# Kernel tuning notes

Measured on AMD Instinct MI355X. Metric: run time of the kernel, lower is better.

## Reference

```python
import jax, jax.numpy as jnp
import numpy as np

N_NODES = 50000
N_EDGES = 800000
IN_DIM = 128
OUT_DIM = 128
CLASS_NUM = 40
EPS = 0.0  # PyG GINConv default eps


def setup_inputs() -> dict:
    key = jax.random.key(0)
    k1, k2, k3, k4 = jax.random.split(key, 4)
    x = jax.random.normal(k1, (N_NODES, IN_DIM), dtype=jnp.float32)
    edge_index = jax.random.randint(k2, (2, N_EDGES), 0, N_NODES, dtype=jnp.int64)
    # Linear(in, out, bias=False) weights, torch layout [out, in]
    W1 = jax.random.normal(k3, (OUT_DIM, IN_DIM), dtype=jnp.float32) / np.sqrt(IN_DIM)
    W2 = jax.random.normal(k4, (CLASS_NUM, OUT_DIM), dtype=jnp.float32) / np.sqrt(OUT_DIM)
    return {"x": x, "edge_index": edge_index, "W1": W1, "W2": W2}


def gin_conv(x, edge_index, W):
    # GINConv: nn((1+eps)*x + sum_{j in N(i)} x_j)
    src, dst = edge_index[0], edge_index[1]
    agg = jax.ops.segment_sum(x[src], dst, num_segments=x.shape[0])  # [N, d]
    h = (1.0 + EPS) * x + agg
    return h @ W.T


def reference(x, edge_index, W1, W2):
    # Layer 1 + relu (dropout is identity at inference, p=0.5 only in training)
    h = jax.nn.relu(gin_conv(x, edge_index, W1))
    # Layer 2 (logits)
    out = gin_conv(h, edge_index, W2)
    return out
```

## Files before the change

kernel.cpp:

```cpp
#include <hip/hip_runtime.h>

#define N_NODES 50000
#define N_EDGES 800000
#define BSHIFT 6
#define NBKT   ((N_NODES + 63) >> BSHIFT)
#define CAP    2048
#define CHUNK_EDGES 4096
#define NBIN_BLOCKS ((N_EDGES + CHUNK_EDGES - 1) / CHUNK_EDGES)
#define NB32   ((N_NODES + 31) / 32)
#define N_PAD  50048
#define GEMM1_NB ((N_NODES + 63) / 64)

typedef __attribute__((ext_vector_type(8))) short short8;
typedef __attribute__((ext_vector_type(4))) float f32x4;

__device__ __forceinline__ int load_idx(const void* ei, int is64, long long pos) {
  return is64 ? (int)((const long long*)ei)[pos] : ((const int*)ei)[pos];
}

__device__ __forceinline__ unsigned bfr(float f) {
  unsigned u = __float_as_uint(f);
  return (u + 0x7FFFu + ((u >> 16) & 1u)) >> 16;
}
__device__ __forceinline__ unsigned bfpk(float lo, float hi) {
  return bfr(lo) | (bfr(hi) << 16);
}
#define ACC_BF4(acc, u)                                                    \
  acc.x += __uint_as_float((u).x << 16);                                   \
  acc.y += __uint_as_float((u).x & 0xffff0000u);                           \
  acc.z += __uint_as_float((u).y << 16);                                   \
  acc.w += __uint_as_float((u).y & 0xffff0000u);

__global__ __launch_bounds__(256) void prep_kernel(const float* __restrict__ W1,
                                                   const float* __restrict__ W2,
                                                   int* __restrict__ resv,
                                                   unsigned short* __restrict__ W1bf,
                                                   unsigned short* __restrict__ W2bf) {
  int b = blockIdx.x, tid = threadIdx.x;
  if (b == 0) {
    ((int4*)resv)[tid] = make_int4(0, 0, 0, 0);
    return;
  }
  int j = (b - 1) * 256 + tid;
  if (j < 128 * 128) {
    W1bf[j] = (unsigned short)bfr(W1[j]);
  } else {
    int jj = j - 128 * 128;
    int c = jj >> 7, k = jj & 127;
    W2bf[jj] = (c < 40) ? (unsigned short)bfr(W2[c * 128 + k]) : 0;
  }
}

__global__ __launch_bounds__(256) void binPlace2_kernel(const void* __restrict__ ei,
                                                        int* __restrict__ resv,
                                                        unsigned* __restrict__ binned) {
  __shared__ int cnt[NBKT];
  __shared__ int lbase[NBKT];
  __shared__ int sflag;
  int tid = threadIdx.x;
  if (tid < 64) {
    const long long* e64 = (const long long*)ei;
    long long v = e64[tid];
    unsigned long long m = __ballot(v >= 0 && v < N_NODES);
    if (tid == 0) sflag = (m == ~0ull) ? 1 : 0;
  }
  for (int i = tid; i < NBKT; i += 256) cnt[i] = 0;
  __syncthreads();
  int f = sflag;
  long long base = (long long)blockIdx.x * CHUNK_EDGES;
  unsigned pk[CHUNK_EDGES / 256];
  #pragma unroll
  for (int it = 0; it < CHUNK_EDGES / 256; ++it) {
    long long e = base + it * 256 + tid;
    unsigned p = 0xFFFFFFFFu;
    if (e < N_EDGES) {
      int src = load_idx(ei, f, e);
      int dst = load_idx(ei, f, (long long)N_EDGES + e);
      int bk = dst >> BSHIFT;
      p = (unsigned)src | ((unsigned)(dst & 63) << 16) | ((unsigned)bk << 22);
      atomicAdd(&cnt[bk], 1);
    }
    pk[it] = p;
  }
  __syncthreads();
  for (int i = tid; i < NBKT; i += 256) {
    int c = cnt[i];
    lbase[i] = c ? (i * CAP + atomicAdd(&resv[i], c)) : 0;
    cnt[i] = 0;
  }
  __syncthreads();
  #pragma unroll
  for (int it = 0; it < CHUNK_EDGES / 256; ++it) {
    unsigned p = pk[it];
    if (p != 0xFFFFFFFFu) {
      int bk = p >> 22;
      int off = atomicAdd(&cnt[bk], 1);
      binned[lbase[bk] + off] = p & 0x3FFFFFu;
    }
  }
}

__global__ __launch_bounds__(256) void csr_gemm1_kernel(const unsigned* __restrict__ binned,
                                                        const int* __restrict__ resv,
                                                        int* __restrict__ rowptr,
                                                        unsigned short* __restrict__ col,
                                                        const float* __restrict__ xin,
                                                        const unsigned short* __restrict__ W1bf,
                                                        unsigned short* __restrict__ Ysbf) {
  __shared__ unsigned short Ysh[64 * 128];
  __shared__ int red[256];
  __shared__ int ncnt[64];
  __shared__ int ncur[64];
  int tid = threadIdx.x;

  if (blockIdx.x < NBKT) {
    int b = blockIdx.x;
    int s = 0;
    for (int i = tid; i < b; i += 256) s += resv[i];
    red[tid] = s;
    __syncthreads();
    #pragma unroll
    for (int off = 128; off > 0; off >>= 1) {
      if (tid < off) red[tid] += red[tid + off];
      __syncthreads();
    }
    int gb = red[0];
    int c = resv[b];
    if (tid < 64) ncnt[tid] = 0;
    if (b == 0 && tid == 0) rowptr[N_NODES] = N_EDGES;
    __syncthreads();
    const unsigned* bb = binned + (size_t)b * CAP;
    for (int i = tid; i < c; i += 256)
      atomicAdd(&ncnt[(bb[i] >> 16) & 63], 1);
    __syncthreads();
    if (tid == 0) {
      int a = gb;
      #pragma unroll
      for (int j = 0; j < 64; ++j) { int t = ncnt[j]; ncur[j] = a; a += t; }
    }
    __syncthreads();
    int node0 = b << BSHIFT;
    if (tid < 64 && node0 + tid < N_NODES) rowptr[node0 + tid] = ncur[tid];
    __syncthreads();
    for (int i = tid; i < c; i += 256) {
      unsigned p = bb[i];
      int slot = atomicAdd(&ncur[(p >> 16) & 63], 1);
      col[slot] = (unsigned short)(p & 0xFFFFu);
    }
    return;
  }

  int wave = tid >> 6, lane = tid & 63;
  int rl = lane & 15, kg = lane >> 4;
  int n0 = (blockIdx.x - NBKT) * 64;
  int rowg = n0 + wave * 16 + rl;
  int row = (rowg < N_NODES) ? rowg : (N_NODES - 1);
  f32x4 acc[8];
  #pragma unroll
  for (int t = 0; t < 8; ++t) acc[t] = (f32x4)(0.f);
  #pragma unroll
  for (int kk = 0; kk < 4; ++kk) {
    int k0 = kk * 32 + kg * 8;
    const float* xr = xin + (size_t)row * 128 + k0;
    float4 a0 = *(const float4*)xr;
    float4 a1 = *(const float4*)(xr + 4);
    short8 a;
    a[0] = (short)bfr(a0.x); a[1] = (short)bfr(a0.y);
    a[2] = (short)bfr(a0.z); a[3] = (short)bfr(a0.w);
    a[4] = (short)bfr(a1.x); a[5] = (short)bfr(a1.y);
    a[6] = (short)bfr(a1.z); a[7] = (short)bfr(a1.w);
    #pragma unroll
    for (int t = 0; t < 8; ++t) {
      short8 b = *(const short8*)(W1bf + (t * 16 + rl) * 128 + k0);
      acc[t] = __builtin_amdgcn_mfma_f32_16x16x32_bf16(a, b, acc[t], 0, 0, 0);
    }
  }
  #pragma unroll
  for (int t = 0; t < 8; ++t) {
    #pragma unroll
    for (int reg = 0; reg < 4; ++reg)
      Ysh[(wave * 16 + kg * 4 + reg) * 128 + t * 16 + rl] =
          (unsigned short)bfr(acc[t][reg]);
  }
  __syncthreads();
  int rows = N_NODES - n0; if (rows > 64) rows = 64;
  uint4* dstb = (uint4*)Ysbf;
  const uint4* srcb = (const uint4*)Ysh;
  for (int i = tid; i < rows * 16; i += 256) {
    int r = i >> 4, j = i & 15;
    int slice = j >> 2, q = j & 3;
    dstb[(size_t)slice * (N_PAD * 4) + (size_t)(n0 + r) * 4 + q] = srcb[i];
  }
}

__global__ __launch_bounds__(256) void gather1_kernel(const unsigned short* __restrict__ Ys,
                                                      const int* __restrict__ rowptr,
                                                      const unsigned short* __restrict__ col,
                                                      unsigned short* __restrict__ h1bf) {
  int bid = blockIdx.x;
  int slice = bid / NB32;
  int nb = bid - slice * NB32;
  int lane = threadIdx.x & 63;
  int wv = threadIdx.x >> 6;
  int g = lane >> 3, s = lane & 7;
  int w = nb * 32 + wv * 8 + g;
  if (w >= N_NODES) return;
  const uint2* Y2 = (const uint2*)(Ys + (size_t)slice * N_PAD * 32);
  float4 acc = make_float4(0.f, 0.f, 0.f, 0.f);
  {
    uint2 u = Y2[(size_t)w * 8 + s];
    ACC_BF4(acc, u);
  }
  int i = rowptr[w], end = rowptr[w + 1];
  for (; i + 3 < end; i += 4) {
    int s0 = col[i], s1 = col[i + 1], s2 = col[i + 2], s3 = col[i + 3];
    uint2 u0 = Y2[(size_t)s0 * 8 + s];
    uint2 u1 = Y2[(size_t)s1 * 8 + s];
    uint2 u2 = Y2[(size_t)s2 * 8 + s];
    uint2 u3 = Y2[(size_t)s3 * 8 + s];
    ACC_BF4(acc, u0); ACC_BF4(acc, u1); ACC_BF4(acc, u2); ACC_BF4(acc, u3);
  }
  for (; i < end; ++i) {
    uint2 u = Y2[(size_t)col[i] * 8 + s];
    ACC_BF4(acc, u);
  }
  uint2 p;
  p.x = bfpk(fmaxf(acc.x, 0.f), fmaxf(acc.y, 0.f));
  p.y = bfpk(fmaxf(acc.z, 0.f), fmaxf(acc.w, 0.f));
  ((uint2*)h1bf)[(size_t)w * 32 + slice * 8 + s] = p;
}

__global__ __launch_bounds__(256) void gather2_kernel(const unsigned short* __restrict__ Zbf,
                                                      const int* __restrict__ rowptr,
                                                      const unsigned short* __restrict__ col,
                                                      float* __restrict__ outp) {
  int lane = threadIdx.x & 63;
  int wv = threadIdx.x >> 6;
  int g = lane >> 3, s = lane & 7;
  int w = blockIdx.x * 32 + wv * 8 + g;
  if (w >= N_NODES) return;
  const uint2* Z2 = (const uint2*)Zbf;
  bool ex = s < 2;
  float4 acc = make_float4(0.f, 0.f, 0.f, 0.f);
  float4 acc2 = make_float4(0.f, 0.f, 0.f, 0.f);
  {
    uint2 u = Z2[(size_t)w * 10 + s];
    ACC_BF4(acc, u);
    if (ex) { uint2 v = Z2[(size_t)w * 10 + 8 + s]; ACC_BF4(acc2, v); }
  }
  int i = rowptr[w], end = rowptr[w + 1];
  for (; i + 1 < end; i += 2) {
    int s0 = col[i], s1 = col[i + 1];
    uint2 u0 = Z2[(size_t)s0 * 10 + s];
    uint2 u1 = Z2[(size_t)s1 * 10 + s];
    ACC_BF4(acc, u0); ACC_BF4(acc, u1);
    if (ex) {
      uint2 v0 = Z2[(size_t)s0 * 10 + 8 + s];
      uint2 v1 = Z2[(size_t)s1 * 10 + 8 + s];
      ACC_BF4(acc2, v0); ACC_BF4(acc2, v1);
    }
  }
  for (; i < end; ++i) {
    int s0 = col[i];
    uint2 u0 = Z2[(size_t)s0 * 10 + s];
    ACC_BF4(acc, u0);
    if (ex) { uint2 v0 = Z2[(size_t)s0 * 10 + 8 + s]; ACC_BF4(acc2, v0); }
  }
  float4* o4 = (float4*)(outp + (size_t)w * 40);
  o4[s] = acc;
  if (ex) o4[8 + s] = acc2;
}

__global__ __launch_bounds__(256) void gemm2_kernel(const unsigned short* __restrict__ h1bf,
                                                    const unsigned short* __restrict__ W2bf,
                                                    unsigned short* __restrict__ Zbf) {
  __shared__ unsigned short Zsh[64 * 40];
  int tid = threadIdx.x;
  int wave = tid >> 6, lane = tid & 63;
  int rl = lane & 15, kg = lane >> 4;
  int n0 = blockIdx.x * 64;
  int rowg = n0 + wave * 16 + rl;
  int row = (rowg < N_NODES) ? rowg : (N_NODES - 1);
  f32x4 acc[3];
  #pragma unroll
  for (int t = 0; t < 3; ++t) acc[t] = (f32x4)(0.f);
  #pragma unroll
  for (int kk = 0; kk < 4; ++kk) {
    int k0 = kk * 32 + kg * 8;
    short8 a = *(const short8*)(h1bf + (size_t)row * 128 + k0);
    #pragma unroll
    for (int t = 0; t < 3; ++t) {
      short8 b = *(const short8*)(W2bf + (t * 16 + rl) * 128 + k0);
      acc[t] = __builtin_amdgcn_mfma_f32_16x16x32_bf16(a, b, acc[t], 0, 0, 0);
    }
  }
  #pragma unroll
  for (int t = 0; t < 3; ++t) {
    int c = t * 16 + rl;
    if (c < 40) {
      #pragma unroll
      for (int reg = 0; reg < 4; ++reg)
        Zsh[(wave * 16 + kg * 4 + reg) * 40 + c] = (unsigned short)bfr(acc[t][reg]);
    }
  }
  __syncthreads();
  int rows = N_NODES - n0; if (rows > 64) rows = 64;
  unsigned* dst = (unsigned*)Zbf + (size_t)n0 * 20;
  const unsigned* src = (const unsigned*)Zsh;
  for (int i = tid; i < rows * 20; i += 256) dst[i] = src[i];
}

extern "C" void kernel_launch(void* const* d_in, const int* in_sizes, int n_in,
                              void* d_out, int out_size, void* d_ws, size_t ws_size,
                              hipStream_t stream) {
  const float* x  = (const float*)d_in[0];
  const void*  ei = d_in[1];
  const float* W1 = (const float*)d_in[2];
  const float* W2 = (const float*)d_in[3];
  float* out = (float*)d_out;

  int* resv   = (int*)d_ws;
  int* rowptr = resv + 1024;
  unsigned* binned = (unsigned*)(rowptr + 50176);
  unsigned short* col  = (unsigned short*)(binned + (size_t)NBKT * CAP);
  unsigned short* Ysbf = col + N_EDGES;
  unsigned short* h1bf = Ysbf + (size_t)4 * N_PAD * 32;
  unsigned short* W1bf = h1bf + (size_t)N_NODES * 128;
  unsigned short* W2bf = W1bf + 128 * 128;
  unsigned short* Zbf  = Ysbf;

  prep_kernel<<<89, 256, 0, stream>>>(W1, W2, resv, W1bf, W2bf);
  binPlace2_kernel<<<NBIN_BLOCKS, 256, 0, stream>>>(ei, resv, binned);
  csr_gemm1_kernel<<<NBKT + GEMM1_NB, 256, 0, stream>>>(binned, resv, rowptr, col,
                                                        x, W1bf, Ysbf);
  gather1_kernel<<<4 * NB32, 256, 0, stream>>>(Ysbf, rowptr, col, h1bf);
  gemm2_kernel<<<GEMM1_NB, 256, 0, stream>>>(h1bf, W2bf, Zbf);
  gather2_kernel<<<NB32, 256, 0, stream>>>(Zbf, rowptr, col, out);
}
```

Baseline: 116.6 us.

## Sort nodes by degree within 128-node buckets to balance gather work

```diff
diff --git a/kernel.cpp b/kernel.cpp
--- a/kernel.cpp
+++ b/kernel.cpp
@@ -2,12 +2,14 @@
 
 #define N_NODES 50000
 #define N_EDGES 800000
-#define BSHIFT 6
-#define NBKT   ((N_NODES + 63) >> BSHIFT)
-#define CAP    2048
+#define BSHIFT 7
+#define BKT_NODES 128
+#define NBKT   ((N_NODES + BKT_NODES - 1) >> BSHIFT)
+#define CAP    4096
 #define CHUNK_EDGES 4096
 #define NBIN_BLOCKS ((N_EDGES + CHUNK_EDGES - 1) / CHUNK_EDGES)
-#define NB32   ((N_NODES + 31) / 32)
+#define NPERM  (NBKT * BKT_NODES)
+#define NB32P  (NPERM / 32)
 #define N_PAD  50048
 #define GEMM1_NB ((N_NODES + 63) / 64)
 
@@ -25,11 +27,11 @@
 __device__ __forceinline__ unsigned bfpk(float lo, float hi) {
   return bfr(lo) | (bfr(hi) << 16);
 }
-#define ACC_BF4(acc, u)                                                    \
+#define ACC_BF4F(acc, u)                                                   \
   acc.x += __uint_as_float((u).x << 16);                                   \
-  acc.y += __uint_as_float((u).x & 0xffff0000u);                           \
+  acc.y += __uint_as_float((u).x);                                         \
   acc.z += __uint_as_float((u).y << 16);                                   \
-  acc.w += __uint_as_float((u).y & 0xffff0000u);
+  acc.w += __uint_as_float((u).y);
 
 __global__ __launch_bounds__(256) void prep_kernel(const float* __restrict__ W1,
                                                    const float* __restrict__ W2,
@@ -77,7 +79,7 @@
       int src = load_idx(ei, f, e);
       int dst = load_idx(ei, f, (long long)N_EDGES + e);
       int bk = dst >> BSHIFT;
-      p = (unsigned)src | ((unsigned)(dst & 63) << 16) | ((unsigned)bk << 22);
+      p = (unsigned)src | ((unsigned)(dst & 127) << 16) | ((unsigned)bk << 23);
       atomicAdd(&cnt[bk], 1);
     }
     pk[it] = p;
@@ -93,9 +95,9 @@
   for (int it = 0; it < CHUNK_EDGES / 256; ++it) {
     unsigned p = pk[it];
     if (p != 0xFFFFFFFFu) {
-      int bk = p >> 22;
+      int bk = p >> 23;
       int off = atomicAdd(&cnt[bk], 1);
-      binned[lbase[bk] + off] = p & 0x3FFFFFu;
+      binned[lbase[bk] + off] = p & 0x7FFFFFu;
     }
   }
 }
@@ -104,13 +106,16 @@
                                                         const int* __restrict__ resv,
                                                         int* __restrict__ rowptr,
                                                         unsigned short* __restrict__ col,
+                                                        unsigned short* __restrict__ permw,
                                                         const float* __restrict__ xin,
                                                         const unsigned short* __restrict__ W1bf,
                                                         unsigned short* __restrict__ Ysbf) {
   __shared__ unsigned short Ysh[64 * 128];
   __shared__ int red[256];
-  __shared__ int ncnt[64];
-  __shared__ int ncur[64];
+  __shared__ int ncnt[BKT_NODES];
+  __shared__ int ncur[BKT_NODES];
+  __shared__ int dcnt[64];
+  __shared__ int dcur[64];
   int tid = threadIdx.x;
 
   if (blockIdx.x < NBKT) {
@@ -126,25 +131,43 @@
     }
     int gb = red[0];
     int c = resv[b];
-    if (tid < 64) ncnt[tid] = 0;
+    if (tid < BKT_NODES) ncnt[tid] = 0;
+    if (tid < 64) dcnt[tid] = 0;
+    if (tid < BKT_NODES) permw[(size_t)b * BKT_NODES + tid] = 0xFFFFu;
     if (b == 0 && tid == 0) rowptr[N_NODES] = N_EDGES;
     __syncthreads();
     const unsigned* bb = binned + (size_t)b * CAP;
     for (int i = tid; i < c; i += 256)
-      atomicAdd(&ncnt[(bb[i] >> 16) & 63], 1);
+      atomicAdd(&ncnt[(bb[i] >> 16) & 127], 1);
     __syncthreads();
     if (tid == 0) {
       int a = gb;
       #pragma unroll
-      for (int j = 0; j < 64; ++j) { int t = ncnt[j]; ncur[j] = a; a += t; }
+      for (int j = 0; j < BKT_NODES; ++j) { int t = ncnt[j]; ncur[j] = a; a += t; }
     }
     __syncthreads();
     int node0 = b << BSHIFT;
-    if (tid < 64 && node0 + tid < N_NODES) rowptr[node0 + tid] = ncur[tid];
-    __syncthreads();
+    int nvalid = N_NODES - node0; if (nvalid > BKT_NODES) nvalid = BKT_NODES;
+    if (tid < nvalid) rowptr[node0 + tid] = ncur[tid];
+    if (tid < nvalid) {
+      int deg = ncnt[tid]; if (deg > 63) deg = 63;
+      atomicAdd(&dcnt[deg], 1);
+    }
+    __syncthreads();
+    if (tid == 0) {
+      int a = 0;
+      #pragma unroll
+      for (int j = 0; j < 64; ++j) { int t = dcnt[j]; dcur[j] = a; a += t; }
+    }
+    __syncthreads();
+    if (tid < nvalid) {
+      int deg = ncnt[tid]; if (deg > 63) deg = 63;
+      int rank = atomicAdd(&dcur[deg], 1);
+      permw[(size_t)b * BKT_NODES + rank] = (unsigned short)(node0 + tid);
+    }
     for (int i = tid; i < c; i += 256) {
       unsigned p = bb[i];
-      int slot = atomicAdd(&ncur[(p >> 16) & 63], 1);
+      int slot = atomicAdd(&ncur[(p >> 16) & 127], 1);
       col[slot] = (unsigned short)(p & 0xFFFFu);
     }
     return;
@@ -196,77 +219,81 @@
 __global__ __launch_bounds__(256) void gather1_kernel(const unsigned short* __restrict__ Ys,
                                                       const int* __restrict__ rowptr,
                                                       const unsigned short* __restrict__ col,
+                                                      const unsigned short* __restrict__ permw,
                                                       unsigned short* __restrict__ h1bf) {
   int bid = blockIdx.x;
-  int slice = bid / NB32;
-  int nb = bid - slice * NB32;
+  int slice = bid / NB32P;
+  int nb = bid - slice * NB32P;
   int lane = threadIdx.x & 63;
   int wv = threadIdx.x >> 6;
   int g = lane >> 3, s = lane & 7;
-  int w = nb * 32 + wv * 8 + g;
-  if (w >= N_NODES) return;
+  int slot = nb * 32 + wv * 8 + g;
+  int node = permw[slot];
+  if (node == 0xFFFF) return;
   const uint2* Y2 = (const uint2*)(Ys + (size_t)slice * N_PAD * 32);
   float4 acc = make_float4(0.f, 0.f, 0.f, 0.f);
   {
-    uint2 u = Y2[(size_t)w * 8 + s];
-    ACC_BF4(acc, u);
-  }
-  int i = rowptr[w], end = rowptr[w + 1];
+    uint2 u = Y2[(size_t)node * 8 + s];
+    ACC_BF4F(acc, u);
+  }
+  int i = rowptr[node], end = rowptr[node + 1];
   for (; i + 3 < end; i += 4) {
     int s0 = col[i], s1 = col[i + 1], s2 = col[i + 2], s3 = col[i + 3];
     uint2 u0 = Y2[(size_t)s0 * 8 + s];
     uint2 u1 = Y2[(size_t)s1 * 8 + s];
     uint2 u2 = Y2[(size_t)s2 * 8 + s];
     uint2 u3 = Y2[(size_t)s3 * 8 + s];
-    ACC_BF4(acc, u0); ACC_BF4(acc, u1); ACC_BF4(acc, u2); ACC_BF4(acc, u3);
+    ACC_BF4F(acc, u0); ACC_BF4F(acc, u1); ACC_BF4F(acc, u2); ACC_BF4F(acc, u3);
   }
   for (; i < end; ++i) {
     uint2 u = Y2[(size_t)col[i] * 8 + s];
-    ACC_BF4(acc, u);
+    ACC_BF4F(acc, u);
   }
   uint2 p;
   p.x = bfpk(fmaxf(acc.x, 0.f), fmaxf(acc.y, 0.f));
   p.y = bfpk(fmaxf(acc.z, 0.f), fmaxf(acc.w, 0.f));
-  ((uint2*)h1bf)[(size_t)w * 32 + slice * 8 + s] = p;
+  ((uint2*)h1bf)[(size_t)node * 32 + slice * 8 + s] = p;
 }
 
 __global__ __launch_bounds__(256) void gather2_kernel(const unsigned short* __restrict__ Zbf,
                                                       const int* __restrict__ rowptr,
                                                       const unsigned short* __restrict__ col,
+                                                      const unsigned short* __restrict__ permw,
                                                       float* __restrict__ outp) {
   int lane = threadIdx.x & 63;
   int wv = threadIdx.x >> 6;
   int g = lane >> 3, s = lane & 7;
-  int w = blockIdx.x * 32 + wv * 8 + g;
-  if (w >= N_NODES) return;
+  int slot = blockIdx.x * 32 + wv * 8 + g;
+  int node = permw[slot];
+  if (node == 0xFFFF) return;
   const uint2* Z2 = (const uint2*)Zbf;
   bool ex = s < 2;
   float4 acc = make_float4(0.f, 0.f, 0.f, 0.f);
   float4 acc2 = make_float4(0.f, 0.f, 0.f, 0.f);
   {
-    uint2 u = Z2[(size_t)w * 10 + s];
-    ACC_BF4(acc, u);
-    if (ex) { uint2 v = Z2[(size_t)w * 10 + 8 + s]; ACC_BF4(acc2, v); }
-  }
-  int i = rowptr[w], end = rowptr[w + 1];
+    uint2 u = Z2[(size_t)node * 10 + s];
+    ACC_BF4F(acc, u);
+    if (ex) { uint2 v = Z2[(size_t)node * 10 + 8 + s]; ACC_BF4F(acc2, v); }
+  }
+  int i = rowptr[node], end = rowptr[node + 1];
   for (; i + 1 < end; i += 2) {
     int s0 = col[i], s1 = col[i + 1];
     uint2 u0 = Z2[(size_t)s0 * 10 + s];
     uint2 u1 = Z2[(size_t)s1 * 10 + s];
-    ACC_BF4(acc, u0); ACC_BF4(acc, u1);
+    ACC_BF4F(acc, u0); ACC_BF4F(acc, u1);
     if (ex) {
       uint2 v0 = Z2[(size_t)s0 * 10 + 8 + s];
       uint2 v1 = Z2[(size_t)s1 * 10 + 8 + s];
-      ACC_BF4(acc2, v0); ACC_BF4(acc2, v1);
+      ACC_BF4F(acc2, v0); ACC_BF4F(acc2, v1);
     }
   }
   for (; i < end; ++i) {
     int s0 = col[i];
     uint2 u0 = Z2[(size_t)s0 * 10 + s];
-    ACC_BF4(acc, u0);
-    if (ex) { uint2 v0 = Z2[(size_t)s0 * 10 + 8 + s]; ACC_BF4(acc2, v0); }
-  }
-  float4* o4 = (float4*)(outp + (size_t)w * 40);
+    ACC_BF4F(acc, u0);
+    if (ex) { uint2 v0 = Z2[(size_t)s0 * 10 + 8 + s]; ACC_BF4F(acc2, v0); }
+  }
+  float4* o4 = (float4*)(outp + (size_t)node * 40);
   o4[s] = acc;
   if (ex) o4[8 + s] = acc2;
 }
@@ -323,7 +350,8 @@
   int* rowptr = resv + 1024;
   unsigned* binned = (unsigned*)(rowptr + 50176);
   unsigned short* col  = (unsigned short*)(binned + (size_t)NBKT * CAP);
-  unsigned short* Ysbf = col + N_EDGES;
+  unsigned short* permw = col + N_EDGES;
+  unsigned short* Ysbf = permw + NPERM;
   unsigned short* h1bf = Ysbf + (size_t)4 * N_PAD * 32;
   unsigned short* W1bf = h1bf + (size_t)N_NODES * 128;
   unsigned short* W2bf = W1bf + 128 * 128;
@@ -332,8 +360,8 @@
   prep_kernel<<<89, 256, 0, stream>>>(W1, W2, resv, W1bf, W2bf);
   binPlace2_kernel<<<NBIN_BLOCKS, 256, 0, stream>>>(ei, resv, binned);
   csr_gemm1_kernel<<<NBKT + GEMM1_NB, 256, 0, stream>>>(binned, resv, rowptr, col,
-                                                        x, W1bf, Ysbf);
-  gather1_kernel<<<4 * NB32, 256, 0, stream>>>(Ysbf, rowptr, col, h1bf);
+                                                        permw, x, W1bf, Ysbf);
+  gather1_kernel<<<4 * NB32P, 256, 0, stream>>>(Ysbf, rowptr, col, permw, h1bf);
   gemm2_kernel<<<GEMM1_NB, 256, 0, stream>>>(h1bf, W2bf, Zbf);
-  gather2_kernel<<<NB32, 256, 0, stream>>>(Zbf, rowptr, col, out);
-}
+  gather2_kernel<<<NB32P, 256, 0, stream>>>(Zbf, rowptr, col, permw, out);
+}
```

New measurement: 117.5 us. About the same (+0.8%).
